# Optimization experiments

Measured on AMD Instinct MI355X. Metric: run time of the kernel, lower is better.

The kernel has to match this reference:

```python
import jax, jax.numpy as jnp
import numpy as np

B, N, D = 8, 256, 128


def setup_inputs() -> dict:
    key = jax.random.key(0)
    ks = jax.random.split(key, 4)
    s1 = 1.0 / np.sqrt(4 * D)
    s2 = 1.0 / np.sqrt(2 * D)
    s3 = 1.0 / np.sqrt(D)
    return {
        "tour_features": jax.random.normal(ks[0], (B, N, D), dtype=jnp.float32),
        "W1": jax.random.uniform(ks[1], (4 * D, 2 * D), jnp.float32, -s1, s1),
        "b1": jnp.zeros((2 * D,), jnp.float32),
        "W2": jax.random.uniform(ks[2], (2 * D, D), jnp.float32, -s2, s2),
        "b2": jnp.zeros((D,), jnp.float32),
        "W3": jax.random.uniform(ks[3], (D, 1), jnp.float32, -s3, s3),
        "b3": jnp.zeros((1,), jnp.float32),
    }


def reference(tour_features, W1, b1, W2, b2, W3, b3):
    Bs, Ns, Ds = tour_features.shape
    x = tour_features
    x_next = jnp.roll(x, -1, axis=1)  # node at (k+1) % N
    # Split first linear's weight by the 4 concatenated feature blocks:
    # cat([x_i, x_{i+1}, x_j, x_{j+1}]) @ W1 == x_i@W1a + x_{i+1}@W1b + x_j@W1c + x_{j+1}@W1d
    W1a, W1b, W1c, W1d = jnp.split(W1, 4, axis=0)
    Pi = x @ W1a + x_next @ W1b          # [B, N, 2D] (i-side projection)
    Pj = x @ W1c + x_next @ W1d          # [B, N, 2D] (j-side projection)
    h1 = jax.nn.relu(Pi[:, :, None, :] + Pj[:, None, :, :] + b1)  # [B, N, N, 2D]
    h2 = jax.nn.relu(h1 @ W2 + b2)       # [B, N, N, D]
    score = jnp.tanh((h2 @ W3 + b3)[..., 0])  # [B, N, N]
    # Valid pairs: j >= i + 2 and not (j - i == N - 1)
    ii = jnp.arange(Ns)[:, None]
    jj = jnp.arange(Ns)[None, :]
    mask = (jj >= ii + 2) & (jj - ii != Ns - 1)
    improvement_matrix = jnp.where(mask[None], score, 0.0)
    improved_tour = jnp.broadcast_to(jnp.arange(Ns), (Bs, Ns))
    return improved_tour, improvement_matrix
```

## Files before the change

kernel.cpp:

```cpp
#include <hip/hip_runtime.h>


typedef __attribute__((ext_vector_type(8))) short short8;
typedef __attribute__((ext_vector_type(8))) _Float16 half8;
typedef __attribute__((ext_vector_type(4))) float floatx4;

static __device__ __forceinline__ unsigned short f2bf(float f) {
  unsigned int x = __float_as_uint(f);
  x += 0x7fff + ((x >> 16) & 1);
  return (unsigned short)(x >> 16);
}

static __device__ __forceinline__ unsigned short f2h(float f) {
  _Float16 h = (_Float16)f;
  return __builtin_bit_cast(unsigned short, h);
}

static __device__ __forceinline__ float fast_tanh(float x) {
  float e = __expf(2.0f * fabsf(x));
  float t = 1.0f - 2.0f * __builtin_amdgcn_rcpf(e + 1.0f);
  return copysignf(t, x);
}

static __device__ __forceinline__ long pack_fp8(half8 s) {
  int lo = __builtin_amdgcn_cvt_pk_fp8_f32((float)s[0], (float)s[1], 0, false);
  lo = __builtin_amdgcn_cvt_pk_fp8_f32((float)s[2], (float)s[3], lo, true);
  int hi = __builtin_amdgcn_cvt_pk_fp8_f32((float)s[4], (float)s[5], 0, false);
  hi = __builtin_amdgcn_cvt_pk_fp8_f32((float)s[6], (float)s[7], hi, true);
  return (long)(unsigned)lo | ((long)hi << 32);
}

static __device__ __forceinline__ void gload_lds16(const void* g, void* l) {
  __builtin_amdgcn_global_load_lds(
      (const __attribute__((address_space(1))) unsigned int*)g,
      (__attribute__((address_space(3))) unsigned int*)l, 16, 0, 0);
}

__global__ __launch_bounds__(256) void k_prep(
    const float* __restrict__ x, const float* __restrict__ W1,
    const float* __restrict__ W2, float* __restrict__ out,
    unsigned char* __restrict__ W2F8, unsigned short* __restrict__ W1T,
    unsigned short* __restrict__ xcat) {
  int e = blockIdx.x * 256 + threadIdx.x;
  if (e < 2048) {
    out[e] = (float)(e & 255);
  } else if (e < 526336) {
    out[e] = 0.f;
  } else if (e < 542720) {
    int t = e - 526336;
    int p = t >> 7, n = t & 127;
    float f0 = W2[(2 * p) * 128 + n] * 16.f;
    float f1 = W2[(2 * p + 1) * 128 + n] * 16.f;
    int v2 = __builtin_amdgcn_cvt_pk_fp8_f32(f0, f1, 0, false);
    int q = n >> 5, which = (n >> 4) & 1, l = n & 15;
    int c = p >> 2, off = (p & 3) * 2;
    int cs = (c & 16) | ((c ^ l) & 15);
    *(unsigned short*)(W2F8 + q * 8192 + l * 512 + cs * 16 + which * 8 + off) =
        (unsigned short)(v2 & 0xffff);
  } else if (e < 673792) {
    int e3 = e - 542720;
    int n = e3 >> 8, k = e3 & 255;
    int v = k >> 3;
    int sw = (((v & 16) | ((v ^ (n & 15)) & 15)) << 3) | (k & 7);
    W1T[(n << 8) + sw] = f2bf(W1[((k + (n & 256)) << 8) + (n & 255)]);
  } else {
    int e4 = e - 673792;
    int r = e4 >> 8, k = e4 & 255;
    int v = k >> 3;
    int sw = (((v & 16) | ((v ^ (r & 15)) & 15)) << 3) | (k & 7);
    int pos = r & 255;
    int pos2 = (k < 128) ? pos : ((pos + 1) & 255);
    xcat[(r << 8) + sw] = f2bf(x[(((r >> 8) << 8) + pos2) * 128 + (k & 127)]);
  }
}

__global__ __launch_bounds__(256) void k_proj(
    const unsigned short* __restrict__ xcat, const unsigned short* __restrict__ W1T,
    const float* __restrict__ b1, unsigned short* __restrict__ PiH,
    unsigned short* __restrict__ PjH) {
  const int mg = blockIdx.x >> 3;
  const int ng = blockIdx.x & 7;
  const int tid = threadIdx.x;
  const int wr = tid >> 6, lane = tid & 63, quad = lane >> 4, l15 = lane & 15;

  __shared__ unsigned short As[64 * 256];
  __shared__ unsigned short Bs[64 * 256];

  const unsigned short* Asrc = xcat + mg * 64 * 256;
  const unsigned short* Bsrc = W1T + ng * 64 * 256;
#pragma unroll
  for (int it = 0; it < 8; ++it) {
    const int c = it * 256 + wr * 64 + lane;
    gload_lds16(Asrc + c * 8, &As[(it * 256 + wr * 64) * 8]);
    gload_lds16(Bsrc + c * 8, &Bs[(it * 256 + wr * 64) * 8]);
  }
  __syncthreads();

  floatx4 acc[4];
#pragma unroll
  for (int mt = 0; mt < 4; ++mt) acc[mt] = (floatx4)0.f;

  const char* Ab = (const char*)As;
  const char* Bb = (const char*)Bs + wr * 16 * 512;
  const int base_sw = l15 * 512 + ((quad ^ l15) << 4);

#pragma unroll
  for (int ks = 0; ks < 8; ++ks) {
    const int swz = base_sw ^ (ks << 6);
    short8 bfr = *(const short8*)(Bb + swz);
#pragma unroll
    for (int mt = 0; mt < 4; ++mt) {
      short8 afr = *(const short8*)(Ab + mt * 8192 + swz);
      acc[mt] = __builtin_amdgcn_mfma_f32_16x16x32_bf16(afr, bfr, acc[mt], 0, 0, 0);
    }
  }

  const int ch = ng * 64 + wr * 16 + l15;
  const float bias = (ch < 256) ? b1[ch] : 0.f;
  const bool isPi = (ch < 256);
  unsigned short* dst = isPi ? PiH : PjH;
  const int chan = ch & 255;
  const int ck = chan >> 3, coff = chan & 7;
#pragma unroll
  for (int mt = 0; mt < 4; ++mt)
#pragma unroll
    for (int r = 0; r < 4; ++r) {
      int row = mg * 64 + mt * 16 + quad * 4 + r;
      int cpos;
      if (isPi) cpos = chan;
      else {
        int cs = (ck & 16) | ((ck ^ (row & 15)) & 15);
        cpos = cs * 8 + coff;
      }
      dst[row * 256 + cpos] = f2h(acc[mt][r] + bias);
    }
}

__global__ __launch_bounds__(256, 3) void k_main(
    const unsigned short* __restrict__ PiH, const unsigned short* __restrict__ PjH,
    const unsigned char* __restrict__ W2F8, const float* __restrict__ b2,
    const float* __restrict__ W3, const float* __restrict__ b3,
    float* __restrict__ outm) {
  const int tid = threadIdx.x;
  const int wr = tid >> 6;
  const int lane = tid & 63, quad = lane >> 4, l15 = lane & 15;

  __shared__ unsigned char W2s[32768];
  __shared__ unsigned char PjS[16384];
  __shared__ unsigned char PiS[4096];

  const int bid = blockIdx.x;
  const int b = bid / 288;
  const int rem = bid - b * 288;
  int jt = 0, basej = 0;
  if (rem >= 8)   { jt = 1; basej = 8;   }
  if (rem >= 24)  { jt = 2; basej = 24;  }
  if (rem >= 48)  { jt = 3; basej = 48;  }
  if (rem >= 80)  { jt = 4; basej = 80;  }
  if (rem >= 120) { jt = 5; basej = 120; }
  if (rem >= 168) { jt = 6; basej = 168; }
  if (rem >= 224) { jt = 7; basej = 224; }
  const int i = (rem - basej) * 4 + wr;

  const unsigned char* pjsrc =
      (const unsigned char*)(PjH + ((b << 8) + jt * 32) * 256);
  const unsigned char* pisrc =
      (const unsigned char*)(PiH + ((b << 8) + i) * 256);
#pragma unroll
  for (int it = 0; it < 8; ++it) {
    const int c = it * 256 + wr * 64 + lane;
    gload_lds16(W2F8 + c * 16, &W2s[(it * 256 + wr * 64) * 16]);
  }
#pragma unroll
  for (int it = 0; it < 4; ++it) {
    const int c = it * 256 + wr * 64 + lane;
    gload_lds16(pjsrc + c * 16, &PjS[(it * 256 + wr * 64) * 16]);
  }
  gload_lds16(pisrc + (lane & 31) * 16, &PiS[wr * 1024]);
  __syncthreads();

  const char* W2base = (const char*)&W2s[0];
  const char* PjBase = (const char*)&PjS[0];
  const char* PiBase = (const char*)&PiS[0] + wr * 1024 + quad * 16;
  const int sw16 = l15 * 512 + (((quad ^ l15) & 15) << 4);

  floatx4 acc[2][8];
#pragma unroll
  for (int mt = 0; mt < 2; ++mt)
#pragma unroll
    for (int nt = 0; nt < 8; ++nt) acc[mt][nt] = (floatx4)0.f;

  union U4 { uint4 v; half8 h; };
  U4 piR[2], pjR[2][2];
  piR[0].v = *(const uint4*)(PiBase);
  pjR[0][0].v = *(const uint4*)(PjBase + sw16);
  pjR[0][1].v = *(const uint4*)(PjBase + 8192 + sw16);

  uint4 bfA[4], bfB[4];
  {
    const char* b0 = W2base + sw16;
#pragma unroll
    for (int q = 0; q < 4; ++q) bfA[q] = *(const uint4*)(b0 + q * 8192);
  }

#pragma unroll
  for (int ks = 0; ks < 8; ++ks) {
    const int cur = ks & 1, nxt = cur ^ 1;
    if (ks < 7) {
      const char* bn = W2base + (sw16 ^ ((ks + 1) << 6));
#pragma unroll
      for (int q = 0; q < 4; ++q)
        ((ks & 1) ? bfA : bfB)[q] = *(const uint4*)(bn + q * 8192);
    }
    if (ks < 7) {
      piR[nxt].v = *(const uint4*)(PiBase + (ks + 1) * 64);
      const char* pj = PjBase + (sw16 ^ ((ks + 1) << 6));
      pjR[nxt][0].v = *(const uint4*)(pj);
      pjR[nxt][1].v = *(const uint4*)(pj + 8192);
    }
    const half8 s0 = __builtin_elementwise_max(piR[cur].h + pjR[cur][0].h,
                                               (half8)(_Float16)0);
    const half8 s1 = __builtin_elementwise_max(piR[cur].h + pjR[cur][1].h,
                                               (half8)(_Float16)0);
    const long a0 = pack_fp8(s0);
    const long a1 = pack_fp8(s1);
    const uint4* bc = (ks & 1) ? bfB : bfA;
    __builtin_amdgcn_s_setprio(1);
#pragma unroll
    for (int q = 0; q < 4; ++q) {
      const long blo = (long)bc[q].x | ((long)bc[q].y << 32);
      const long bhi = (long)bc[q].z | ((long)bc[q].w << 32);
      acc[0][2 * q]     = __builtin_amdgcn_mfma_f32_16x16x32_fp8_fp8(a0, blo, acc[0][2 * q], 0, 0, 0);
      acc[1][2 * q]     = __builtin_amdgcn_mfma_f32_16x16x32_fp8_fp8(a1, blo, acc[1][2 * q], 0, 0, 0);
      acc[0][2 * q + 1] = __builtin_amdgcn_mfma_f32_16x16x32_fp8_fp8(a0, bhi, acc[0][2 * q + 1], 0, 0, 0);
      acc[1][2 * q + 1] = __builtin_amdgcn_mfma_f32_16x16x32_fp8_fp8(a1, bhi, acc[1][2 * q + 1], 0, 0, 0);
    }
    __builtin_amdgcn_s_setprio(0);
  }

  float* orow = outm + ((b << 8) + i) * 256 + jt * 32;
  const float b3v = b3[0];
  const float s16 = 0.0625f;
#pragma unroll
  for (int mt = 0; mt < 2; ++mt) {
    float p0 = 0, p1 = 0, p2 = 0, p3 = 0;
#pragma unroll
    for (int nt = 0; nt < 8; ++nt) {
      float w3v = W3[nt * 16 + l15];
      float b2v = b2[nt * 16 + l15];
      floatx4 a = acc[mt][nt];
      p0 += fmaxf(fmaf(a[0], s16, b2v), 0.f) * w3v;
      p1 += fmaxf(fmaf(a[1], s16, b2v), 0.f) * w3v;
      p2 += fmaxf(fmaf(a[2], s16, b2v), 0.f) * w3v;
      p3 += fmaxf(fmaf(a[3], s16, b2v), 0.f) * w3v;
    }
#pragma unroll
    for (int m = 8; m >= 1; m >>= 1) {
      p0 += __shfl_xor(p0, m, 16);
      p1 += __shfl_xor(p1, m, 16);
      p2 += __shfl_xor(p2, m, 16);
      p3 += __shfl_xor(p3, m, 16);
    }
    if (l15 == 0) {
      const int jl = jt * 32 + mt * 16 + quad * 4;
      float ps[4] = {p0, p1, p2, p3};
#pragma unroll
      for (int r = 0; r < 4; ++r) {
        int j = jl + r;
        float sc = fast_tanh(ps[r] + b3v);
        bool valid = (j >= i + 2) && (j - i != 255);
        orow[mt * 16 + quad * 4 + r] = valid ? sc : 0.f;
      }
    }
  }
}

extern "C" void kernel_launch(void* const* d_in, const int* in_sizes, int n_in,
                              void* d_out, int out_size, void* d_ws, size_t ws_size,
                              hipStream_t stream) {
  const float* x  = (const float*)d_in[0];
  const float* W1 = (const float*)d_in[1];
  const float* b1 = (const float*)d_in[2];
  const float* W2 = (const float*)d_in[3];
  const float* b2 = (const float*)d_in[4];
  const float* W3 = (const float*)d_in[5];
  const float* b3 = (const float*)d_in[6];
  float* out = (float*)d_out;

  unsigned short* PiH  = (unsigned short*)d_ws;
  unsigned short* PjH  = PiH + 524288;
  unsigned short* W1T  = PjH + 524288;
  unsigned short* xcat = W1T + 131072;
  unsigned char*  W2F8 = (unsigned char*)(xcat + 524288);

  k_prep<<<4680, 256, 0, stream>>>(x, W1, W2, out, W2F8, W1T, xcat);
  k_proj<<<256, 256, 0, stream>>>(xcat, W1T, b1, PiH, PjH);
  k_main<<<2304, 256, 0, stream>>>(PiH, PjH, W2F8, b2, W3, b3, out + 2048);
}
```

Baseline: 96.96 us.

## Process two rows per wave in main kernel and move output/W2 prep into proj

Each wave in k_main now computes two i rows against the same 32-column j tile, so the block count is halved and every W2 and Pj fragment loaded from LDS feeds twice as many MFMAs. Occupancy is lowered to 2 blocks per SM to leave room for the doubled accumulators. Separately, the output zeroing and W2 fp8 conversion move out of k_prep into extra blocks of k_proj, so that work runs alongside the projection GEMM. The risks are higher register pressure and fewer blocks available to hide latency.

```diff
diff --git a/kernel.cpp b/kernel.cpp
--- a/kernel.cpp
+++ b/kernel.cpp
@@ -38,33 +38,15 @@
 
 __global__ __launch_bounds__(256) void k_prep(
     const float* __restrict__ x, const float* __restrict__ W1,
-    const float* __restrict__ W2, float* __restrict__ out,
-    unsigned char* __restrict__ W2F8, unsigned short* __restrict__ W1T,
-    unsigned short* __restrict__ xcat) {
+    unsigned short* __restrict__ W1T, unsigned short* __restrict__ xcat) {
   int e = blockIdx.x * 256 + threadIdx.x;
-  if (e < 2048) {
-    out[e] = (float)(e & 255);
-  } else if (e < 526336) {
-    out[e] = 0.f;
-  } else if (e < 542720) {
-    int t = e - 526336;
-    int p = t >> 7, n = t & 127;
-    float f0 = W2[(2 * p) * 128 + n] * 16.f;
-    float f1 = W2[(2 * p + 1) * 128 + n] * 16.f;
-    int v2 = __builtin_amdgcn_cvt_pk_fp8_f32(f0, f1, 0, false);
-    int q = n >> 5, which = (n >> 4) & 1, l = n & 15;
-    int c = p >> 2, off = (p & 3) * 2;
-    int cs = (c & 16) | ((c ^ l) & 15);
-    *(unsigned short*)(W2F8 + q * 8192 + l * 512 + cs * 16 + which * 8 + off) =
-        (unsigned short)(v2 & 0xffff);
-  } else if (e < 673792) {
-    int e3 = e - 542720;
-    int n = e3 >> 8, k = e3 & 255;
+  if (e < 131072) {
+    int n = e >> 8, k = e & 255;
     int v = k >> 3;
     int sw = (((v & 16) | ((v ^ (n & 15)) & 15)) << 3) | (k & 7);
     W1T[(n << 8) + sw] = f2bf(W1[((k + (n & 256)) << 8) + (n & 255)]);
   } else {
-    int e4 = e - 673792;
+    int e4 = e - 131072;
     int r = e4 >> 8, k = e4 & 255;
     int v = k >> 3;
     int sw = (((v & 16) | ((v ^ (r & 15)) & 15)) << 3) | (k & 7);
@@ -77,10 +59,33 @@
 __global__ __launch_bounds__(256) void k_proj(
     const unsigned short* __restrict__ xcat, const unsigned short* __restrict__ W1T,
     const float* __restrict__ b1, unsigned short* __restrict__ PiH,
-    unsigned short* __restrict__ PjH) {
+    unsigned short* __restrict__ PjH, const float* __restrict__ W2,
+    float* __restrict__ out, unsigned char* __restrict__ W2F8) {
+  const int tid = threadIdx.x;
+
+  if (blockIdx.x >= 256) {
+    int e = (blockIdx.x - 256) * 256 + tid;
+    if (e < 2048) {
+      out[e] = (float)(e & 255);
+    } else if (e < 526336) {
+      out[e] = 0.f;
+    } else if (e < 542720) {
+      int t = e - 526336;
+      int p = t >> 7, n = t & 127;
+      float f0 = W2[(2 * p) * 128 + n] * 16.f;
+      float f1 = W2[(2 * p + 1) * 128 + n] * 16.f;
+      int v2 = __builtin_amdgcn_cvt_pk_fp8_f32(f0, f1, 0, false);
+      int q = n >> 5, which = (n >> 4) & 1, l = n & 15;
+      int c = p >> 2, off = (p & 3) * 2;
+      int cs = (c & 16) | ((c ^ l) & 15);
+      *(unsigned short*)(W2F8 + q * 8192 + l * 512 + cs * 16 + which * 8 + off) =
+          (unsigned short)(v2 & 0xffff);
+    }
+    return;
+  }
+
   const int mg = blockIdx.x >> 3;
   const int ng = blockIdx.x & 7;
-  const int tid = threadIdx.x;
   const int wr = tid >> 6, lane = tid & 63, quad = lane >> 4, l15 = lane & 15;
 
   __shared__ unsigned short As[64 * 256];
@@ -136,7 +141,7 @@
     }
 }
 
-__global__ __launch_bounds__(256, 3) void k_main(
+__global__ __launch_bounds__(256, 2) void k_main(
     const unsigned short* __restrict__ PiH, const unsigned short* __restrict__ PjH,
     const unsigned char* __restrict__ W2F8, const float* __restrict__ b2,
     const float* __restrict__ W3, const float* __restrict__ b3,
@@ -150,22 +155,23 @@
   __shared__ unsigned char PiS[4096];
 
   const int bid = blockIdx.x;
-  const int b = bid / 288;
-  const int rem = bid - b * 288;
+  const int b = bid / 144;
+  const int rem = bid - b * 144;
   int jt = 0, basej = 0;
-  if (rem >= 8)   { jt = 1; basej = 8;   }
-  if (rem >= 24)  { jt = 2; basej = 24;  }
-  if (rem >= 48)  { jt = 3; basej = 48;  }
-  if (rem >= 80)  { jt = 4; basej = 80;  }
-  if (rem >= 120) { jt = 5; basej = 120; }
-  if (rem >= 168) { jt = 6; basej = 168; }
-  if (rem >= 224) { jt = 7; basej = 224; }
-  const int i = (rem - basej) * 4 + wr;
+  if (rem >= 4)   { jt = 1; basej = 4;   }
+  if (rem >= 12)  { jt = 2; basej = 12;  }
+  if (rem >= 24)  { jt = 3; basej = 24;  }
+  if (rem >= 40)  { jt = 4; basej = 40;  }
+  if (rem >= 60)  { jt = 5; basej = 60;  }
+  if (rem >= 84)  { jt = 6; basej = 84;  }
+  if (rem >= 112) { jt = 7; basej = 112; }
+  const int i0 = (rem - basej) * 8 + wr * 2;
 
   const unsigned char* pjsrc =
       (const unsigned char*)(PjH + ((b << 8) + jt * 32) * 256);
   const unsigned char* pisrc =
-      (const unsigned char*)(PiH + ((b << 8) + i) * 256);
+      (const unsigned char*)(PiH + ((b << 8) + i0 + (lane >> 5)) * 256) +
+      (lane & 31) * 16;
 #pragma unroll
   for (int it = 0; it < 8; ++it) {
     const int c = it * 256 + wr * 64 + lane;
@@ -176,7 +182,7 @@
     const int c = it * 256 + wr * 64 + lane;
     gload_lds16(pjsrc + c * 16, &PjS[(it * 256 + wr * 64) * 16]);
   }
-  gload_lds16(pisrc + (lane & 31) * 16, &PiS[wr * 1024]);
+  gload_lds16(pisrc, &PiS[wr * 1024]);
   __syncthreads();
 
   const char* W2base = (const char*)&W2s[0];
@@ -184,15 +190,18 @@
   const char* PiBase = (const char*)&PiS[0] + wr * 1024 + quad * 16;
   const int sw16 = l15 * 512 + (((quad ^ l15) & 15) << 4);
 
-  floatx4 acc[2][8];
-#pragma unroll
-  for (int mt = 0; mt < 2; ++mt)
-#pragma unroll
-    for (int nt = 0; nt < 8; ++nt) acc[mt][nt] = (floatx4)0.f;
+  floatx4 acc[2][2][8];
+#pragma unroll
+  for (int is = 0; is < 2; ++is)
+#pragma unroll
+    for (int mt = 0; mt < 2; ++mt)
+#pragma unroll
+      for (int nt = 0; nt < 8; ++nt) acc[is][mt][nt] = (floatx4)0.f;
 
   union U4 { uint4 v; half8 h; };
-  U4 piR[2], pjR[2][2];
-  piR[0].v = *(const uint4*)(PiBase);
+  U4 piR[2][2], pjR[2][2];
+  piR[0][0].v = *(const uint4*)(PiBase);
+  piR[0][1].v = *(const uint4*)(PiBase + 512);
   pjR[0][0].v = *(const uint4*)(PjBase + sw16);
   pjR[0][1].v = *(const uint4*)(PjBase + 8192 + sw16);
 
@@ -213,63 +222,76 @@
         ((ks & 1) ? bfA : bfB)[q] = *(const uint4*)(bn + q * 8192);
     }
     if (ks < 7) {
-      piR[nxt].v = *(const uint4*)(PiBase + (ks + 1) * 64);
+      piR[nxt][0].v = *(const uint4*)(PiBase + (ks + 1) * 64);
+      piR[nxt][1].v = *(const uint4*)(PiBase + 512 + (ks + 1) * 64);
       const char* pj = PjBase + (sw16 ^ ((ks + 1) << 6));
       pjR[nxt][0].v = *(const uint4*)(pj);
       pjR[nxt][1].v = *(const uint4*)(pj + 8192);
     }
-    const half8 s0 = __builtin_elementwise_max(piR[cur].h + pjR[cur][0].h,
-                                               (half8)(_Float16)0);
-    const half8 s1 = __builtin_elementwise_max(piR[cur].h + pjR[cur][1].h,
-                                               (half8)(_Float16)0);
-    const long a0 = pack_fp8(s0);
-    const long a1 = pack_fp8(s1);
+    const half8 s00 = __builtin_elementwise_max(piR[cur][0].h + pjR[cur][0].h,
+                                                (half8)(_Float16)0);
+    const half8 s01 = __builtin_elementwise_max(piR[cur][0].h + pjR[cur][1].h,
+                                                (half8)(_Float16)0);
+    const half8 s10 = __builtin_elementwise_max(piR[cur][1].h + pjR[cur][0].h,
+                                                (half8)(_Float16)0);
+    const half8 s11 = __builtin_elementwise_max(piR[cur][1].h + pjR[cur][1].h,
+                                                (half8)(_Float16)0);
+    const long a00 = pack_fp8(s00), a01 = pack_fp8(s01);
+    const long a10 = pack_fp8(s10), a11 = pack_fp8(s11);
     const uint4* bc = (ks & 1) ? bfB : bfA;
     __builtin_amdgcn_s_setprio(1);
 #pragma unroll
     for (int q = 0; q < 4; ++q) {
       const long blo = (long)bc[q].x | ((long)bc[q].y << 32);
       const long bhi = (long)bc[q].z | ((long)bc[q].w << 32);
-      acc[0][2 * q]     = __builtin_amdgcn_mfma_f32_16x16x32_fp8_fp8(a0, blo, acc[0][2 * q], 0, 0, 0);
-      acc[1][2 * q]     = __builtin_amdgcn_mfma_f32_16x16x32_fp8_fp8(a1, blo, acc[1][2 * q], 0, 0, 0);
-      acc[0][2 * q + 1] = __builtin_amdgcn_mfma_f32_16x16x32_fp8_fp8(a0, bhi, acc[0][2 * q + 1], 0, 0, 0);
-      acc[1][2 * q + 1] = __builtin_amdgcn_mfma_f32_16x16x32_fp8_fp8(a1, bhi, acc[1][2 * q + 1], 0, 0, 0);
+      acc[0][0][2 * q]     = __builtin_amdgcn_mfma_f32_16x16x32_fp8_fp8(a00, blo, acc[0][0][2 * q], 0, 0, 0);
+      acc[0][1][2 * q]     = __builtin_amdgcn_mfma_f32_16x16x32_fp8_fp8(a01, blo, acc[0][1][2 * q], 0, 0, 0);
+      acc[1][0][2 * q]     = __builtin_amdgcn_mfma_f32_16x16x32_fp8_fp8(a10, blo, acc[1][0][2 * q], 0, 0, 0);
+      acc[1][1][2 * q]     = __builtin_amdgcn_mfma_f32_16x16x32_fp8_fp8(a11, blo, acc[1][1][2 * q], 0, 0, 0);
+      acc[0][0][2 * q + 1] = __builtin_amdgcn_mfma_f32_16x16x32_fp8_fp8(a00, bhi, acc[0][0][2 * q + 1], 0, 0, 0);
+      acc[0][1][2 * q + 1] = __builtin_amdgcn_mfma_f32_16x16x32_fp8_fp8(a01, bhi, acc[0][1][2 * q + 1], 0, 0, 0);
+      acc[1][0][2 * q + 1] = __builtin_amdgcn_mfma_f32_16x16x32_fp8_fp8(a10, bhi, acc[1][0][2 * q + 1], 0, 0, 0);
+      acc[1][1][2 * q + 1] = __builtin_amdgcn_mfma_f32_16x16x32_fp8_fp8(a11, bhi, acc[1][1][2 * q + 1], 0, 0, 0);
     }
     __builtin_amdgcn_s_setprio(0);
   }
 
-  float* orow = outm + ((b << 8) + i) * 256 + jt * 32;
   const float b3v = b3[0];
   const float s16 = 0.0625f;
 #pragma unroll
-  for (int mt = 0; mt < 2; ++mt) {
-    float p0 = 0, p1 = 0, p2 = 0, p3 = 0;
-#pragma unroll
-    for (int nt = 0; nt < 8; ++nt) {
-      float w3v = W3[nt * 16 + l15];
-      float b2v = b2[nt * 16 + l15];
-      floatx4 a = acc[mt][nt];
-      p0 += fmaxf(fmaf(a[0], s16, b2v), 0.f) * w3v;
-      p1 += fmaxf(fmaf(a[1], s16, b2v), 0.f) * w3v;
-      p2 += fmaxf(fmaf(a[2], s16, b2v), 0.f) * w3v;
-      p3 += fmaxf(fmaf(a[3], s16, b2v), 0.f) * w3v;
-    }
-#pragma unroll
-    for (int m = 8; m >= 1; m >>= 1) {
-      p0 += __shfl_xor(p0, m, 16);
-      p1 += __shfl_xor(p1, m, 16);
-      p2 += __shfl_xor(p2, m, 16);
-      p3 += __shfl_xor(p3, m, 16);
-    }
-    if (l15 == 0) {
-      const int jl = jt * 32 + mt * 16 + quad * 4;
-      float ps[4] = {p0, p1, p2, p3};
-#pragma unroll
-      for (int r = 0; r < 4; ++r) {
-        int j = jl + r;
-        float sc = fast_tanh(ps[r] + b3v);
-        bool valid = (j >= i + 2) && (j - i != 255);
-        orow[mt * 16 + quad * 4 + r] = valid ? sc : 0.f;
+  for (int is = 0; is < 2; ++is) {
+    const int i = i0 + is;
+    float* orow = outm + ((b << 8) + i) * 256 + jt * 32;
+#pragma unroll
+    for (int mt = 0; mt < 2; ++mt) {
+      float p0 = 0, p1 = 0, p2 = 0, p3 = 0;
+#pragma unroll
+      for (int nt = 0; nt < 8; ++nt) {
+        float w3v = W3[nt * 16 + l15];
+        float b2v = b2[nt * 16 + l15];
+        floatx4 a = acc[is][mt][nt];
+        p0 += fmaxf(fmaf(a[0], s16, b2v), 0.f) * w3v;
+        p1 += fmaxf(fmaf(a[1], s16, b2v), 0.f) * w3v;
+        p2 += fmaxf(fmaf(a[2], s16, b2v), 0.f) * w3v;
+        p3 += fmaxf(fmaf(a[3], s16, b2v), 0.f) * w3v;
+      }
+#pragma unroll
+      for (int m = 8; m >= 1; m >>= 1) {
+        p0 += __shfl_xor(p0, m, 16);
+        p1 += __shfl_xor(p1, m, 16);
+        p2 += __shfl_xor(p2, m, 16);
+        p3 += __shfl_xor(p3, m, 16);
+      }
+      if (l15 == 0) {
+        const int jl = jt * 32 + mt * 16 + quad * 4;
+        float ps[4] = {p0, p1, p2, p3};
+#pragma unroll
+        for (int r = 0; r < 4; ++r) {
+          int j = jl + r;
+          float sc = fast_tanh(ps[r] + b3v);
+          bool valid = (j >= i + 2) && (j - i != 255);
+          orow[mt * 16 + quad * 4 + r] = valid ? sc : 0.f;
+        }
       }
     }
   }
@@ -293,7 +315,7 @@
   unsigned short* xcat = W1T + 131072;
   unsigned char*  W2F8 = (unsigned char*)(xcat + 524288);
 
-  k_prep<<<4680, 256, 0, stream>>>(x, W1, W2, out, W2F8, W1T, xcat);
-  k_proj<<<256, 256, 0, stream>>>(xcat, W1T, b1, PiH, PjH);
-  k_main<<<2304, 256, 0, stream>>>(PiH, PjH, W2F8, b2, W3, b3, out + 2048);
-}
+  k_prep<<<2560, 256, 0, stream>>>(x, W1, W1T, xcat);
+  k_proj<<<2376, 256, 0, stream>>>(xcat, W1T, b1, PiH, PjH, W2, out, W2F8);
+  k_main<<<1152, 256, 0, stream>>>(PiH, PjH, W2F8, b2, W3, b3, out + 2048);
+}
```

Result: slower. 99.46 us (+2.6%).
